# Kernel tuning notes

Measured on AMD Instinct MI355X. Metric: run time of the kernel, lower is better.

## Reference

```python
import jax, jax.numpy as jnp
import numpy as np

N_HEAD = 16
D_HEAD = 64
D_MODEL = 1024
SCALE = 1.0 / float(D_HEAD) ** 0.5
LN_EPS = 1e-5


def _rel_shift(x):
    # x: [b, n, i, j] -> Transformer-XL relative shift
    b, n, i, j = x.shape
    x = jnp.pad(x, ((0, 0), (0, 0), (0, 0), (1, 0)))  # zero-pad front of last dim
    x = x.reshape(b, n, j + 1, i)[:, :, 1:, :]
    return x.reshape(b, n, i, j)


def _layer_norm(x, g, b):
    mu = jnp.mean(x, axis=-1, keepdims=True)
    var = jnp.mean(jnp.square(x - mu), axis=-1, keepdims=True)
    return g * (x - mu) / jnp.sqrt(var + LN_EPS) + b


def setup_inputs() -> dict:
    key = jax.random.key(0)
    ks = jax.random.split(key, 8)
    qlen, bsz = 1024, 4
    w = jax.random.normal(ks[0], (qlen, bsz, D_MODEL), jnp.float32)
    r = jax.random.normal(ks[1], (qlen, D_MODEL), jnp.float32)
    r_w_bias = 0.02 * jax.random.normal(ks[2], (N_HEAD, D_HEAD), jnp.float32)
    r_r_bias = 0.02 * jax.random.normal(ks[3], (N_HEAD, D_HEAD), jnp.float32)
    attn_mask = jnp.triu(jnp.ones((qlen, qlen), bool), 1)  # causal, True = masked
    qkv_w = 0.02 * jax.random.normal(ks[4], (D_MODEL, 3 * N_HEAD * D_HEAD), jnp.float32)
    qkv_b = jnp.zeros((3 * N_HEAD * D_HEAD,), jnp.float32)
    rk_w = 0.02 * jax.random.normal(ks[5], (D_MODEL, N_HEAD * D_HEAD), jnp.float32)
    rk_b = jnp.zeros((N_HEAD * D_HEAD,), jnp.float32)
    o_w = 0.02 * jax.random.normal(ks[6], (N_HEAD * D_HEAD, D_MODEL), jnp.float32)
    o_b = jnp.zeros((D_MODEL,), jnp.float32)
    ln_g = jnp.ones((D_MODEL,), jnp.float32)
    ln_b = jnp.zeros((D_MODEL,), jnp.float32)
    return {"w": w, "r": r, "r_w_bias": r_w_bias, "r_r_bias": r_r_bias,
            "qkv_w": qkv_w, "qkv_b": qkv_b, "rk_w": rk_w, "rk_b": rk_b,
            "o_w": o_w, "o_b": o_b, "ln_g": ln_g, "ln_b": ln_b,
            "attn_mask": attn_mask}


def reference(w, r, r_w_bias, r_r_bias, qkv_w, qkv_b, rk_w, rk_b, o_w, o_b, ln_g, ln_b, attn_mask):
    qlen, bsz, _ = w.shape
    # post-lnorm path (pre_lnorm=False)
    heads = w @ qkv_w + qkv_b                       # [q, b, 3*H*D]
    q, k, v = jnp.split(heads, 3, axis=-1)
    q = q.reshape(qlen, bsz, N_HEAD, D_HEAD)
    k = k.reshape(qlen, bsz, N_HEAD, D_HEAD)
    v = v.reshape(qlen, bsz, N_HEAD, D_HEAD)
    rk = (r @ rk_w + rk_b).reshape(-1, N_HEAD, D_HEAD)  # [rlen, H, D]
    AC = jnp.einsum('ibnd,jbnd->bnij', q + r_w_bias, k)
    BD = _rel_shift(jnp.einsum('ibnd,jnd->bnij', q + r_r_bias, rk))
    score = SCALE * (AC + BD)                       # [b, H, q, k]
    score = jnp.where(attn_mask[None, None, :, :], -jnp.inf, score)
    prob = jax.nn.softmax(score, axis=-1)
    vec = jnp.einsum('bnij,jbnd->ibnd', prob, v).reshape(qlen, bsz, N_HEAD * D_HEAD)
    attn_out = vec @ o_w + o_b
    return _layer_norm(w + attn_out, ln_g, ln_b)
```

## Files before the change

kernel.cpp:

```cpp
#include <hip/hip_runtime.h>
#include <math.h>

#define QL 1024
#define BSZ 4
#define NH 16
#define DH 64
#define DM 1024
#define SCALE_F 0.125f

typedef __attribute__((ext_vector_type(8))) short bf16x8;
typedef __attribute__((ext_vector_type(4))) float f32x4;

__device__ __forceinline__ unsigned short f2bf(float f) {
  union { float f; unsigned int u; } c; c.f = f;
  unsigned int u = c.u;
  u += 0x7FFFu + ((u >> 16) & 1u);
  return (unsigned short)(u >> 16);
}
__device__ __forceinline__ float bf2f(unsigned short u) {
  union { unsigned int i; float f; } c; c.i = ((unsigned int)u) << 16;
  return c.f;
}

__device__ __forceinline__ void ld_lds16(const unsigned short* g, unsigned short* l) {
  __builtin_amdgcn_global_load_lds(
      (const __attribute__((address_space(1))) unsigned int*)g,
      (__attribute__((address_space(3))) unsigned int*)l, 16, 0, 0);
}

__device__ __forceinline__ bf16x8 frag64(const unsigned short* lds, int n, int s) {
  return *(const bf16x8*)(lds + n * 64 + ((s ^ (n & 7)) * 8));
}

template <int CTRL>
__device__ __forceinline__ float dpp_mv(float x) {
  return __int_as_float(__builtin_amdgcn_update_dpp(
      0, __float_as_int(x), CTRL, 0xf, 0xf, true));
}
__device__ __forceinline__ float rowsum16(float x) {
  x += dpp_mv<0x121>(x);
  x += dpp_mv<0x122>(x);
  x += dpp_mv<0x124>(x);
  x += dpp_mv<0x128>(x);
  return x;
}

__global__ __launch_bounds__(256) void prep_kernel(
    const float* __restrict__ w, const float* __restrict__ r,
    const float* __restrict__ qkv_w, const float* __restrict__ rk_w,
    const float* __restrict__ o_w,
    unsigned short* __restrict__ wb, unsigned short* __restrict__ rb,
    unsigned short* __restrict__ qkv_wt, unsigned short* __restrict__ rk_wt,
    unsigned short* __restrict__ o_wt, float* __restrict__ drk) {
  __shared__ __align__(16) unsigned short t[64][72];
  const int bid = blockIdx.x, tid = threadIdx.x;
  if (bid >= 3840) {
    int idx = (bid - 3840) * 256 + tid;
    ((float4*)drk)[idx] = make_float4(0.f, 0.f, 0.f, 0.f);
    return;
  }
  if (bid < 2560) {
    const float* in = (bid < 2048) ? w : r;
    unsigned short* out = (bid < 2048) ? wb : rb;
    int idx = ((bid < 2048) ? bid : (bid - 2048)) * 256 + tid;
    float4 a = *(const float4*)(in + (size_t)idx * 8);
    float4 b = *(const float4*)(in + (size_t)idx * 8 + 4);
    unsigned short o[8] = {f2bf(a.x), f2bf(a.y), f2bf(a.z), f2bf(a.w),
                           f2bf(b.x), f2bf(b.y), f2bf(b.z), f2bf(b.w)};
    *(uint4*)(out + (size_t)idx * 8) = *(const uint4*)o;
    return;
  }
  const float* in; unsigned short* out; int N, n0, k0;
  if (bid < 3328) {
    int l = bid - 2560; in = qkv_w; out = qkv_wt; N = 3072;
    n0 = (l % 48) * 64; k0 = (l / 48) * 64;
  } else if (bid < 3584) {
    int l = bid - 3328; in = rk_w; out = rk_wt; N = 1024;
    n0 = (l & 15) * 64; k0 = (l >> 4) * 64;
  } else {
    int l = bid - 3584; in = o_w; out = o_wt; N = 1024;
    n0 = (l & 15) * 64; k0 = (l >> 4) * 64;
  }
  for (int f = tid; f < 1024; f += 256) {
    int rr = f >> 4, c4 = (f & 15) * 4;
    float4 v = *(const float4*)(in + (size_t)(k0 + rr) * N + n0 + c4);
    t[c4 + 0][rr] = f2bf(v.x); t[c4 + 1][rr] = f2bf(v.y);
    t[c4 + 2][rr] = f2bf(v.z); t[c4 + 3][rr] = f2bf(v.w);
  }
  __syncthreads();
  for (int f = tid; f < 512; f += 256) {
    int rr = f >> 3, seg = (f & 7) * 8;
    *(uint4*)(out + (size_t)(n0 + rr) * 1024 + k0 + seg) = *(const uint4*)&t[rr][seg];
  }
}

__global__ __launch_bounds__(512) void gemm12(
    const unsigned short* __restrict__ wb, const unsigned short* __restrict__ rb,
    const unsigned short* __restrict__ qkv_wt, const unsigned short* __restrict__ rk_wt,
    const float* __restrict__ qkv_b, const float* __restrict__ rk_b,
    const float* __restrict__ rwb, const float* __restrict__ rrb,
    unsigned short* __restrict__ qbf, unsigned short* __restrict__ kbf,
    unsigned short* __restrict__ vtb, unsigned short* __restrict__ rkbf,
    float* __restrict__ drk) {
  __shared__ __align__(16) unsigned short As[2 * 4096];
  __shared__ __align__(16) unsigned short Bs[2 * 4096];
  const int bid = blockIdx.x, tid = threadIdx.x;
  const int w = tid >> 6, lane = tid & 63;
  const int quad = lane >> 4, l15 = lane & 15;
  const int wr = w >> 2, wc = w & 3;
  const bool job0 = bid < 768;
  const unsigned short *A, *BT;
  const float* bias;
  int bm, bn;
  if (job0) {
    A = wb; BT = qkv_wt; bias = qkv_b;
    bn = (bid % 24) * 128; bm = (bid / 24) * 128;
  } else {
    int l = bid - 768;
    A = rb; BT = rk_wt; bias = rk_b;
    bn = (l & 7) * 128; bm = (l >> 3) * 128;
  }
  const int srow = w * 16 + (lane >> 2);
  const int sseg = (lane & 3) ^ ((lane >> 2) & 3);
  f32x4 acc[4][2] = {};

  auto stage = [&](int bf, int k0) {
    ld_lds16(A + (size_t)(bm + srow) * 1024 + k0 + sseg * 8, As + bf * 4096 + w * 512);
    ld_lds16(BT + (size_t)(bn + srow) * 1024 + k0 + sseg * 8, Bs + bf * 4096 + w * 512);
  };

  int buf = 0;
  stage(0, 0);
  for (int k0 = 0; k0 < 1024; k0 += 32) {
    __syncthreads();
    if (k0 + 32 < 1024) stage(buf ^ 1, k0 + 32);
    const unsigned short* Al = As + buf * 4096;
    const unsigned short* Bl = Bs + buf * 4096;
    const int sa = quad ^ (l15 & 3);
    bf16x8 af[4], bfr[2];
#pragma unroll
    for (int rt = 0; rt < 4; ++rt)
      af[rt] = *(const bf16x8*)&Al[(wr * 64 + rt * 16 + l15) * 32 + sa * 8];
#pragma unroll
    for (int nt = 0; nt < 2; ++nt)
      bfr[nt] = *(const bf16x8*)&Bl[(wc * 32 + nt * 16 + l15) * 32 + sa * 8];
#pragma unroll
    for (int rt = 0; rt < 4; ++rt)
#pragma unroll
      for (int nt = 0; nt < 2; ++nt)
        acc[rt][nt] = __builtin_amdgcn_mfma_f32_16x16x32_bf16(af[rt], bfr[nt], acc[rt][nt], 0, 0, 0);
    buf ^= 1;
  }

  if (job0) {
#pragma unroll
    for (int rt = 0; rt < 4; ++rt)
#pragma unroll
      for (int nt = 0; nt < 2; ++nt) {
        int gc = bn + wc * 32 + nt * 16 + l15;
        float bv = bias[gc];
        int part = gc >> 10, h = (gc >> 6) & 15, d = gc & 63;
#pragma unroll
        for (int reg = 0; reg < 4; ++reg) {
          int gr = bm + wr * 64 + rt * 16 + quad * 4 + reg;
          float val = acc[rt][nt][reg] + bv;
          int i = gr >> 2, b = gr & 3;
          if (part == 0)
            qbf[((size_t)((b * NH + h) * QL + i)) * DH + d] = f2bf(val);
          else if (part == 1)
            kbf[((size_t)((b * NH + h) * QL + i)) * DH + d] = f2bf(val);
          else
            vtb[((size_t)((b * NH + h) * DH + d)) * QL + i] = f2bf(val);
        }
      }
  } else {
    const int h = (bn + wc * 32) >> 6;
    float df[2];
#pragma unroll
    for (int nt = 0; nt < 2; ++nt) {
      int dd = (wc & 1) * 32 + nt * 16 + l15;
      df[nt] = rrb[h * DH + dd] - rwb[h * DH + dd];
    }
#pragma unroll
    for (int rt = 0; rt < 4; ++rt) {
      float s[4] = {0.f, 0.f, 0.f, 0.f};
#pragma unroll
      for (int nt = 0; nt < 2; ++nt) {
        int gc = bn + wc * 32 + nt * 16 + l15;
        float bv = bias[gc];
        int d = gc & 63;
#pragma unroll
        for (int reg = 0; reg < 4; ++reg) {
          int gr = bm + wr * 64 + rt * 16 + quad * 4 + reg;
          float val = acc[rt][nt][reg] + bv;
          rkbf[((size_t)(h * QL + gr)) * DH + d] = f2bf(val);
          s[reg] += val * df[nt];
        }
      }
#pragma unroll
      for (int reg = 0; reg < 4; ++reg) {
        float v = s[reg];
        v += __shfl_xor(v, 1);
        v += __shfl_xor(v, 2);
        v += __shfl_xor(v, 4);
        v += __shfl_xor(v, 8);
        if (l15 == 0) {
          int j = bm + wr * 64 + rt * 16 + quad * 4 + reg;
          atomicAdd(&drk[h * QL + j], v);
        }
      }
    }
  }
}

__global__ __launch_bounds__(512) void gemm_o(
    const unsigned short* __restrict__ A, const unsigned short* __restrict__ BT,
    const float* __restrict__ bias, float* __restrict__ Cf) {
  __shared__ __align__(16) unsigned short As[2 * 4096];
  __shared__ __align__(16) unsigned short Bs[2 * 2048];
  const int tid = threadIdx.x;
  const int w = tid >> 6, lane = tid & 63;
  const int quad = lane >> 4, l15 = lane & 15;
  const int wr = w >> 1, wc = w & 1;
  const int bm = blockIdx.y * 128, bn = blockIdx.x * 64;
  const int srow = w * 16 + (lane >> 2);
  const int sseg = (lane & 3) ^ ((lane >> 2) & 3);
  f32x4 acc[2][2] = {};

  auto stage = [&](int bf, int k0) {
    ld_lds16(A + (size_t)(bm + srow) * 1024 + k0 + sseg * 8, As + bf * 4096 + w * 512);
    if (w < 4)
      ld_lds16(BT + (size_t)(bn + srow) * 1024 + k0 + sseg * 8, Bs + bf * 2048 + w * 512);
  };

  int buf = 0;
  stage(0, 0);
  for (int k0 = 0; k0 < 1024; k0 += 32) {
    __syncthreads();
    if (k0 + 32 < 1024) stage(buf ^ 1, k0 + 32);
    const unsigned short* Al = As + buf * 4096;
    const unsigned short* Bl = Bs + buf * 2048;
    const int sa = quad ^ (l15 & 3);
    bf16x8 af[2], bfr[2];
#pragma unroll
    for (int rt = 0; rt < 2; ++rt)
      af[rt] = *(const bf16x8*)&Al[(wr * 32 + rt * 16 + l15) * 32 + sa * 8];
#pragma unroll
    for (int nt = 0; nt < 2; ++nt)
      bfr[nt] = *(const bf16x8*)&Bl[(wc * 32 + nt * 16 + l15) * 32 + sa * 8];
#pragma unroll
    for (int rt = 0; rt < 2; ++rt)
#pragma unroll
      for (int nt = 0; nt < 2; ++nt)
        acc[rt][nt] = __builtin_amdgcn_mfma_f32_16x16x32_bf16(af[rt], bfr[nt], acc[rt][nt], 0, 0, 0);
    buf ^= 1;
  }

#pragma unroll
  for (int rt = 0; rt < 2; ++rt)
#pragma unroll
    for (int nt = 0; nt < 2; ++nt) {
      int gc = bn + wc * 32 + nt * 16 + l15;
      float bv = bias[gc];
#pragma unroll
      for (int reg = 0; reg < 4; ++reg) {
        int gr = bm + wr * 32 + rt * 16 + quad * 4 + reg;
        Cf[(size_t)gr * DM + gc] = acc[rt][nt][reg] + bv;
      }
    }
}

__global__ __launch_bounds__(256, 4) void attn_kernel(
    const unsigned short* __restrict__ qbf, const unsigned short* __restrict__ kbf,
    const unsigned short* __restrict__ vtb, const unsigned short* __restrict__ rkb,
    const float* __restrict__ drk, const float* __restrict__ rwb,
    unsigned short* __restrict__ vecb) {
  __shared__ __align__(16) unsigned short SH[20480];
  unsigned short* Ks = SH;
  unsigned short* Vs = SH + 8192;
  unsigned short* PM = SH + 16384;

  const int tid = threadIdx.x;
  const int wg = tid >> 6, lane = tid & 63;
  const int quad = lane >> 4, l15 = lane & 15;
  const int bh = blockIdx.x, b = bh >> 4, h = bh & 15;
  const int y = 15 - (int)blockIdx.y;
  const int i0 = y * 64, tS = y, T = y + 1;

  const unsigned short* kB0 = kbf + (size_t)bh * QL * DH;
  const unsigned short* vB0 = vtb + (size_t)bh * DH * QL;
  const unsigned short* rB0 = rkb + (size_t)h * QL * DH;
  const float* drkh = drk + h * QL;
  unsigned short* pmw = PM + wg * 1024;

  const int srow8 = lane >> 3, sseg8 = lane & 7;

  bf16x8 qf[2];
  {
    int qrow = i0 + wg * 16 + l15;
    const unsigned short* qp = qbf + ((size_t)bh * QL + qrow) * DH;
#pragma unroll
    for (int s = 0; s < 2; ++s) {
      int off = s * 32 + quad * 8;
      uint4 raw = *(const uint4*)(qp + off);
      const unsigned short* ru = (const unsigned short*)&raw;
      float4 wb0 = *(const float4*)(rwb + h * DH + off);
      float4 wb1 = *(const float4*)(rwb + h * DH + off + 4);
      union { bf16x8 v; unsigned short u[8]; } qc;
      qc.u[0] = f2bf(bf2f(ru[0]) + wb0.x); qc.u[1] = f2bf(bf2f(ru[1]) + wb0.y);
      qc.u[2] = f2bf(bf2f(ru[2]) + wb0.z); qc.u[3] = f2bf(bf2f(ru[3]) + wb0.w);
      qc.u[4] = f2bf(bf2f(ru[4]) + wb1.x); qc.u[5] = f2bf(bf2f(ru[5]) + wb1.y);
      qc.u[6] = f2bf(bf2f(ru[6]) + wb1.z); qc.u[7] = f2bf(bf2f(ru[7]) + wb1.w);
      qf[s] = qc.v;
    }
  }

  auto rel_frag = [&](int gb, f32x4& c) {
    int row = min(gb + l15, QL - 1);
    const unsigned short* rp = rB0 + (size_t)row * DH;
    f32x4 a = {0.f, 0.f, 0.f, 0.f};
    a = __builtin_amdgcn_mfma_f32_16x16x32_bf16(qf[0], *(const bf16x8*)(rp + quad * 8), a, 0, 0, 0);
    a = __builtin_amdgcn_mfma_f32_16x16x32_bf16(qf[1], *(const bf16x8*)(rp + 32 + quad * 8), a, 0, 0, 0);
    float dv = drkh[row];
    a[0] += dv; a[1] += dv; a[2] += dv; a[3] += dv;
    c = a;
  };

  auto stage_tile = [&](int t, int buf) {
    const unsigned short* kb = kB0 + (size_t)(t * 64) * DH;
    const unsigned short* vb = vB0 + t * 64;
    unsigned short* kd = Ks + buf * 4096;
    unsigned short* vd = Vs + buf * 4096;
#pragma unroll
    for (int ii = 0; ii < 2; ++ii) {
      int row = wg * 16 + ii * 8 + srow8;
      int gs = sseg8 ^ (row & 7);
      ld_lds16(kb + (size_t)row * DH + gs * 8, kd + (wg * 16 + ii * 8) * 64);
      ld_lds16(vb + (size_t)row * QL + gs * 8, vd + (wg * 16 + ii * 8) * 64);
    }
  };

  float lrow[4] = {0.f, 0.f, 0.f, 0.f};
  f32x4 pv[4];
#pragma unroll
  for (int r = 0; r < 4; ++r) pv[r] = (f32x4){0.f, 0.f, 0.f, 0.f};

  f32x4 rc[5];
  {
    const int Bt0 = 1008 - i0 - 16 * wg;
#pragma unroll
    for (int f = 0; f < 5; ++f) rel_frag(Bt0 + 16 * f, rc[f]);
  }

  int buf = 0;
  stage_tile(0, 0);
  for (int t = 0; t < T; ++t) {
    __syncthreads();
    if (t + 1 < T) stage_tile(t + 1, buf ^ 1);
    const bool diag = (t == tS);
    const unsigned short* ksl = Ks + buf * 4096;
    const unsigned short* vsl = Vs + buf * 4096;

    f32x4 sacc[4];
#pragma unroll
    for (int nt = 0; nt < 4; ++nt) {
      int n = nt * 16 + l15;
      f32x4 c = {0.f, 0.f, 0.f, 0.f};
      c = __builtin_amdgcn_mfma_f32_16x16x32_bf16(qf[0], frag64(ksl, n, quad), c, 0, 0, 0);
      c = __builtin_amdgcn_mfma_f32_16x16x32_bf16(qf[1], frag64(ksl, n, 4 + quad), c, 0, 0, 0);
      sacc[nt] = c;
    }

#pragma unroll
    for (int r = 0; r < 4; ++r) {
      const int il = wg * 16 + quad * 4 + r;
      const int ls = l15 + 15 - quad * 4 - r;
      const int srcl = (quad << 4) | (ls & 15);
      float rot[5];
#pragma unroll
      for (int f = 0; f < 5; ++f) rot[f] = __shfl(rc[f][r], srcl, 64);
      const bool lo = ls < 16;
      float psum = 0.f;
      const int prow = quad * 4 + r;
      const int psw = prow & 7;
#pragma unroll
      for (int nt = 0; nt < 4; ++nt) {
        float band = lo ? rot[nt] : rot[nt + 1];
        float s = (sacc[nt][r] + band) * SCALE_F;
        if (diag && (nt * 16 + l15) > il) s = -1e30f;
        float e = __expf(s);
        psum += e;
        int jl = nt * 16 + l15;
        pmw[prow * 64 + (((jl >> 3) ^ psw) << 3) + (jl & 7)] = f2bf(e);
      }
      lrow[r] += rowsum16(psum);
    }

    bf16x8 pf0 = frag64(pmw, l15, quad);
    bf16x8 pf1 = frag64(pmw, l15, 4 + quad);
#pragma unroll
    for (int nt = 0; nt < 4; ++nt) {
      int n = nt * 16 + l15;
      pv[nt] = __builtin_amdgcn_mfma_f32_16x16x32_bf16(pf0, frag64(vsl, n, quad), pv[nt], 0, 0, 0);
      pv[nt] = __builtin_amdgcn_mfma_f32_16x16x32_bf16(pf1, frag64(vsl, n, 4 + quad), pv[nt], 0, 0, 0);
    }

    if (t + 1 < T) {
      rc[0] = rc[4];
      const int Bt = 1008 - i0 + 64 * (t + 1) - 16 * wg;
#pragma unroll
      for (int f = 1; f < 5; ++f) rel_frag(Bt + 16 * f, rc[f]);
    }
    buf ^= 1;
  }

#pragma unroll
  for (int nt = 0; nt < 4; ++nt)
#pragma unroll
    for (int r = 0; r < 4; ++r) {
      int il = wg * 16 + quad * 4 + r;
      float val = pv[nt][r] / lrow[r];
      vecb[((size_t)((i0 + il) * BSZ + b)) * DM + h * DH + nt * 16 + l15] = f2bf(val);
    }
}

__global__ __launch_bounds__(256) void ln_kernel(
    const float* __restrict__ w, const float* __restrict__ attn,
    const float* __restrict__ g, const float* __restrict__ bta,
    float* __restrict__ out) {
  __shared__ float red[4];
  __shared__ float sval[2];
  const int row = blockIdx.x, tid = threadIdx.x;
  const float* wr = w + (size_t)row * DM;
  const float* ar = attn + (size_t)row * DM;
  float4 wv = *(const float4*)(wr + tid * 4);
  float4 av = *(const float4*)(ar + tid * 4);
  float x0 = wv.x + av.x, x1 = wv.y + av.y, x2 = wv.z + av.z, x3 = wv.w + av.w;
  float s = x0 + x1 + x2 + x3;
#pragma unroll
  for (int off = 32; off; off >>= 1) s += __shfl_down(s, off, 64);
  const int lane = tid & 63, wvi = tid >> 6;
  if (lane == 0) red[wvi] = s;
  __syncthreads();
  if (tid == 0) sval[0] = (red[0] + red[1] + red[2] + red[3]) * (1.0f / 1024.0f);
  __syncthreads();
  const float mu = sval[0];
  float d0 = x0 - mu, d1 = x1 - mu, d2 = x2 - mu, d3 = x3 - mu;
  float vs2 = d0 * d0 + d1 * d1 + d2 * d2 + d3 * d3;
#pragma unroll
  for (int off = 32; off; off >>= 1) vs2 += __shfl_down(vs2, off, 64);
  if (lane == 0) red[wvi] = vs2;
  __syncthreads();
  if (tid == 0)
    sval[1] = rsqrtf((red[0] + red[1] + red[2] + red[3]) * (1.0f / 1024.0f) + 1e-5f);
  __syncthreads();
  const float inv = sval[1];
  float4 gv = *(const float4*)(g + tid * 4);
  float4 bv = *(const float4*)(bta + tid * 4);
  float4 ov;
  ov.x = gv.x * d0 * inv + bv.x;
  ov.y = gv.y * d1 * inv + bv.y;
  ov.z = gv.z * d2 * inv + bv.z;
  ov.w = gv.w * d3 * inv + bv.w;
  *(float4*)(out + (size_t)row * DM + tid * 4) = ov;
}

extern "C" void kernel_launch(void* const* d_in, const int* in_sizes, int n_in,
                              void* d_out, int out_size, void* d_ws, size_t ws_size,
                              hipStream_t stream) {
  const float* w     = (const float*)d_in[0];
  const float* r     = (const float*)d_in[1];
  const float* rwb   = (const float*)d_in[2];
  const float* rrb   = (const float*)d_in[3];
  const float* qkv_w = (const float*)d_in[4];
  const float* qkv_b = (const float*)d_in[5];
  const float* rk_w  = (const float*)d_in[6];
  const float* rk_b  = (const float*)d_in[7];
  const float* o_w   = (const float*)d_in[8];
  const float* o_b   = (const float*)d_in[9];
  const float* ln_g  = (const float*)d_in[10];
  const float* ln_b  = (const float*)d_in[11];

  float* out = (float*)d_out;
  char* p = (char*)d_ws;
  unsigned short* wb     = (unsigned short*)p; p += (size_t)4096 * 1024 * 2;
  unsigned short* rb     = (unsigned short*)p; p += (size_t)1024 * 1024 * 2;
  unsigned short* qkv_wt = (unsigned short*)p; p += (size_t)3072 * 1024 * 2;
  unsigned short* rk_wt  = (unsigned short*)p; p += (size_t)1024 * 1024 * 2;
  unsigned short* o_wt   = (unsigned short*)p; p += (size_t)1024 * 1024 * 2;
  unsigned short* qbf    = (unsigned short*)p; p += (size_t)BSZ * NH * QL * DH * 2;
  unsigned short* kbf    = (unsigned short*)p; p += (size_t)BSZ * NH * QL * DH * 2;
  unsigned short* vtb    = (unsigned short*)p; p += (size_t)BSZ * NH * QL * DH * 2;
  unsigned short* rkbf   = (unsigned short*)p; p += (size_t)NH * QL * DH * 2;
  float*          drk    = (float*)p;          p += (size_t)NH * QL * 4;
  unsigned short* vecb   = (unsigned short*)p; p += (size_t)4096 * 1024 * 2;
  float*          attnf  = (float*)p;          p += (size_t)4096 * 1024 * 4;

  prep_kernel<<<3856, 256, 0, stream>>>(w, r, qkv_w, rk_w, o_w,
                                        wb, rb, qkv_wt, rk_wt, o_wt, drk);
  gemm12<<<832, 512, 0, stream>>>(wb, rb, qkv_wt, rk_wt, qkv_b, rk_b, rwb, rrb,
                                  qbf, kbf, vtb, rkbf, drk);
  attn_kernel<<<dim3(64, 16), 256, 0, stream>>>(qbf, kbf, vtb, rkbf, drk, rwb, vecb);
  gemm_o<<<dim3(16, 32), 512, 0, stream>>>(vecb, o_wt, o_b, attnf);
  ln_kernel<<<4096, 256, 0, stream>>>(w, attnf, ln_g, ln_b, out);
}
```

Measured before the change: 280.9 us.

## Widen QKV GEMM tiles to 128x256 and prefetch rel-pos fragments in attention

The fused QKV/rk GEMM now computes 128x256 output tiles per block (4x4 MFMA accumulators per wave), which halves the grid and raises arithmetic intensity per LDS load. In the attention kernel, the relative-position key rows for the next tile are loaded into registers one iteration ahead and converted with MFMA at the start of the following iteration, hiding global load latency behind compute. The costs are higher register and LDS use per block, which may lower occupancy, and a grid of 416 blocks may leave CUs unevenly loaded.

```diff
diff --git a/kernel.cpp b/kernel.cpp
--- a/kernel.cpp
+++ b/kernel.cpp
@@ -103,30 +103,33 @@
     unsigned short* __restrict__ vtb, unsigned short* __restrict__ rkbf,
     float* __restrict__ drk) {
   __shared__ __align__(16) unsigned short As[2 * 4096];
-  __shared__ __align__(16) unsigned short Bs[2 * 4096];
+  __shared__ __align__(16) unsigned short Bs[2 * 8192];
   const int bid = blockIdx.x, tid = threadIdx.x;
   const int w = tid >> 6, lane = tid & 63;
   const int quad = lane >> 4, l15 = lane & 15;
   const int wr = w >> 2, wc = w & 3;
-  const bool job0 = bid < 768;
+  const bool job0 = bid < 384;
   const unsigned short *A, *BT;
   const float* bias;
   int bm, bn;
   if (job0) {
     A = wb; BT = qkv_wt; bias = qkv_b;
-    bn = (bid % 24) * 128; bm = (bid / 24) * 128;
+    bn = (bid % 12) * 256; bm = (bid / 12) * 128;
   } else {
-    int l = bid - 768;
+    int l = bid - 384;
     A = rb; BT = rk_wt; bias = rk_b;
-    bn = (l & 7) * 128; bm = (l >> 3) * 128;
-  }
-  const int srow = w * 16 + (lane >> 2);
-  const int sseg = (lane & 3) ^ ((lane >> 2) & 3);
-  f32x4 acc[4][2] = {};
+    bn = (l & 3) * 256; bm = (l >> 2) * 128;
+  }
+  const int srow = tid >> 2;
+  const int sseg = (tid & 3) ^ (srow & 3);
+  f32x4 acc[4][4] = {};
 
   auto stage = [&](int bf, int k0) {
     ld_lds16(A + (size_t)(bm + srow) * 1024 + k0 + sseg * 8, As + bf * 4096 + w * 512);
-    ld_lds16(BT + (size_t)(bn + srow) * 1024 + k0 + sseg * 8, Bs + bf * 4096 + w * 512);
+#pragma unroll
+    for (int i = 0; i < 2; ++i)
+      ld_lds16(BT + (size_t)(bn + i * 128 + srow) * 1024 + k0 + sseg * 8,
+               Bs + bf * 8192 + i * 4096 + w * 512);
   };
 
   int buf = 0;
@@ -135,19 +138,19 @@
     __syncthreads();
     if (k0 + 32 < 1024) stage(buf ^ 1, k0 + 32);
     const unsigned short* Al = As + buf * 4096;
-    const unsigned short* Bl = Bs + buf * 4096;
+    const unsigned short* Bl = Bs + buf * 8192;
     const int sa = quad ^ (l15 & 3);
-    bf16x8 af[4], bfr[2];
+    bf16x8 af[4], bfr[4];
 #pragma unroll
     for (int rt = 0; rt < 4; ++rt)
       af[rt] = *(const bf16x8*)&Al[(wr * 64 + rt * 16 + l15) * 32 + sa * 8];
 #pragma unroll
-    for (int nt = 0; nt < 2; ++nt)
-      bfr[nt] = *(const bf16x8*)&Bl[(wc * 32 + nt * 16 + l15) * 32 + sa * 8];
+    for (int nt = 0; nt < 4; ++nt)
+      bfr[nt] = *(const bf16x8*)&Bl[(wc * 64 + nt * 16 + l15) * 32 + sa * 8];
 #pragma unroll
     for (int rt = 0; rt < 4; ++rt)
 #pragma unroll
-      for (int nt = 0; nt < 2; ++nt)
+      for (int nt = 0; nt < 4; ++nt)
         acc[rt][nt] = __builtin_amdgcn_mfma_f32_16x16x32_bf16(af[rt], bfr[nt], acc[rt][nt], 0, 0, 0);
     buf ^= 1;
   }
@@ -156,8 +159,8 @@
 #pragma unroll
     for (int rt = 0; rt < 4; ++rt)
 #pragma unroll
-      for (int nt = 0; nt < 2; ++nt) {
-        int gc = bn + wc * 32 + nt * 16 + l15;
+      for (int nt = 0; nt < 4; ++nt) {
+        int gc = bn + wc * 64 + nt * 16 + l15;
         float bv = bias[gc];
         int part = gc >> 10, h = (gc >> 6) & 15, d = gc & 63;
 #pragma unroll
@@ -174,21 +177,20 @@
         }
       }
   } else {
-    const int h = (bn + wc * 32) >> 6;
-    float df[2];
-#pragma unroll
-    for (int nt = 0; nt < 2; ++nt) {
-      int dd = (wc & 1) * 32 + nt * 16 + l15;
+    const int h = (bn + wc * 64) >> 6;
+    float df[4];
+#pragma unroll
+    for (int nt = 0; nt < 4; ++nt) {
+      int dd = nt * 16 + l15;
       df[nt] = rrb[h * DH + dd] - rwb[h * DH + dd];
     }
 #pragma unroll
     for (int rt = 0; rt < 4; ++rt) {
       float s[4] = {0.f, 0.f, 0.f, 0.f};
 #pragma unroll
-      for (int nt = 0; nt < 2; ++nt) {
-        int gc = bn + wc * 32 + nt * 16 + l15;
-        float bv = bias[gc];
-        int d = gc & 63;
+      for (int nt = 0; nt < 4; ++nt) {
+        int d = nt * 16 + l15;
+        float bv = bias[h * DH + d];
 #pragma unroll
         for (int reg = 0; reg < 4; ++reg) {
           int gr = bm + wr * 64 + rt * 16 + quad * 4 + reg;
@@ -315,17 +317,6 @@
     }
   }
 
-  auto rel_frag = [&](int gb, f32x4& c) {
-    int row = min(gb + l15, QL - 1);
-    const unsigned short* rp = rB0 + (size_t)row * DH;
-    f32x4 a = {0.f, 0.f, 0.f, 0.f};
-    a = __builtin_amdgcn_mfma_f32_16x16x32_bf16(qf[0], *(const bf16x8*)(rp + quad * 8), a, 0, 0, 0);
-    a = __builtin_amdgcn_mfma_f32_16x16x32_bf16(qf[1], *(const bf16x8*)(rp + 32 + quad * 8), a, 0, 0, 0);
-    float dv = drkh[row];
-    a[0] += dv; a[1] += dv; a[2] += dv; a[3] += dv;
-    c = a;
-  };
-
   auto stage_tile = [&](int t, int buf) {
     const unsigned short* kb = kB0 + (size_t)(t * 64) * DH;
     const unsigned short* vb = vB0 + t * 64;
@@ -346,10 +337,46 @@
   for (int r = 0; r < 4; ++r) pv[r] = (f32x4){0.f, 0.f, 0.f, 0.f};
 
   f32x4 rc[5];
+  bf16x8 rraw0[4], rraw1[4];
+  float rdrk[4];
+
+  auto rel_load = [&](int tnext) {
+    const int Bt = 1008 - i0 + 64 * tnext - 16 * wg;
+#pragma unroll
+    for (int f = 0; f < 4; ++f) {
+      int row = min(Bt + 16 * (f + 1) + l15, QL - 1);
+      const unsigned short* rp = rB0 + (size_t)row * DH;
+      rraw0[f] = *(const bf16x8*)(rp + quad * 8);
+      rraw1[f] = *(const bf16x8*)(rp + 32 + quad * 8);
+      rdrk[f] = drkh[row];
+    }
+  };
+  auto rel_convert = [&]() {
+    rc[0] = rc[4];
+#pragma unroll
+    for (int f = 0; f < 4; ++f) {
+      f32x4 a = {0.f, 0.f, 0.f, 0.f};
+      a = __builtin_amdgcn_mfma_f32_16x16x32_bf16(qf[0], rraw0[f], a, 0, 0, 0);
+      a = __builtin_amdgcn_mfma_f32_16x16x32_bf16(qf[1], rraw1[f], a, 0, 0, 0);
+      float dv = rdrk[f];
+      a[0] += dv; a[1] += dv; a[2] += dv; a[3] += dv;
+      rc[f + 1] = a;
+    }
+  };
+
   {
     const int Bt0 = 1008 - i0 - 16 * wg;
 #pragma unroll
-    for (int f = 0; f < 5; ++f) rel_frag(Bt0 + 16 * f, rc[f]);
+    for (int f = 0; f < 5; ++f) {
+      int row = min(Bt0 + 16 * f + l15, QL - 1);
+      const unsigned short* rp = rB0 + (size_t)row * DH;
+      f32x4 a = {0.f, 0.f, 0.f, 0.f};
+      a = __builtin_amdgcn_mfma_f32_16x16x32_bf16(qf[0], *(const bf16x8*)(rp + quad * 8), a, 0, 0, 0);
+      a = __builtin_amdgcn_mfma_f32_16x16x32_bf16(qf[1], *(const bf16x8*)(rp + 32 + quad * 8), a, 0, 0, 0);
+      float dv = drkh[row];
+      a[0] += dv; a[1] += dv; a[2] += dv; a[3] += dv;
+      rc[f] = a;
+    }
   }
 
   int buf = 0;
@@ -357,6 +384,8 @@
   for (int t = 0; t < T; ++t) {
     __syncthreads();
     if (t + 1 < T) stage_tile(t + 1, buf ^ 1);
+    if (t > 0) rel_convert();
+    if (t + 1 < T) rel_load(t + 1);
     const bool diag = (t == tS);
     const unsigned short* ksl = Ks + buf * 4096;
     const unsigned short* vsl = Vs + buf * 4096;
@@ -403,13 +432,6 @@
       int n = nt * 16 + l15;
       pv[nt] = __builtin_amdgcn_mfma_f32_16x16x32_bf16(pf0, frag64(vsl, n, quad), pv[nt], 0, 0, 0);
       pv[nt] = __builtin_amdgcn_mfma_f32_16x16x32_bf16(pf1, frag64(vsl, n, 4 + quad), pv[nt], 0, 0, 0);
-    }
-
-    if (t + 1 < T) {
-      rc[0] = rc[4];
-      const int Bt = 1008 - i0 + 64 * (t + 1) - 16 * wg;
-#pragma unroll
-      for (int f = 1; f < 5; ++f) rel_frag(Bt + 16 * f, rc[f]);
     }
     buf ^= 1;
   }
@@ -498,7 +520,7 @@
 
   prep_kernel<<<3856, 256, 0, stream>>>(w, r, qkv_w, rk_w, o_w,
                                         wb, rb, qkv_wt, rk_wt, o_wt, drk);
-  gemm12<<<832, 512, 0, stream>>>(wb, rb, qkv_wt, rk_wt, qkv_b, rk_b, rwb, rrb,
+  gemm12<<<416, 512, 0, stream>>>(wb, rb, qkv_wt, rk_wt, qkv_b, rk_b, rwb, rrb,
                                   qbf, kbf, vtb, rkbf, drk);
   attn_kernel<<<dim3(64, 16), 256, 0, stream>>>(qbf, kbf, vtb, rkbf, drk, rwb, vecb);
   gemm_o<<<dim3(16, 32), 512, 0, stream>>>(vecb, o_wt, o_b, attnf);
```

After: 307.9 us. 1.1x slower.
